# Performance work log

Hardware: AMD Instinct MI355X
Metric: run time of the kernel (lower is better)

The kernel has to match this reference:

```python
import jax, jax.numpy as jnp
import numpy as np
from jax import lax

C = 128          # channel_size
NUM_HEAD = 2
P = 4            # local_patch_num


def setup_inputs() -> dict:
    key = jax.random.key(0)
    ks = jax.random.split(key, 16)
    def w(k, shape, scale=0.02):
        return jax.random.normal(k, shape, dtype=jnp.float32) * scale
    return dict(
        x=jax.random.normal(ks[0], (16, C, 128, 128), jnp.float32),
        h0=jax.random.normal(ks[1], (1, C, 64, 64), jnp.float32),
        c0=jax.random.normal(ks[2], (1, C, 64, 64), jnp.float32),
        conv_w=w(ks[3], (C, C, 2, 2)), conv_b=jnp.zeros((C,), jnp.float32),
        qkv1_w=w(ks[4], (3 * C, C)), qkv1_b=jnp.zeros((3 * C,), jnp.float32),
        mlp1_w1=w(ks[5], (4 * C, C)), mlp1_b1=jnp.zeros((4 * C,), jnp.float32),
        mlp1_w2=w(ks[6], (C, 4 * C)), mlp1_b2=jnp.zeros((C,), jnp.float32),
        qkv2_w=w(ks[7], (3 * C, C)), qkv2_b=jnp.zeros((3 * C,), jnp.float32),
        mlp2_w1=w(ks[8], (4 * C, C)), mlp2_b1=jnp.zeros((4 * C,), jnp.float32),
        mlp2_w2=w(ks[9], (C, 4 * C)), mlp2_b2=jnp.zeros((C,), jnp.float32),
        lstm_wx=w(ks[10], (4 * C, C)),   # 1x1 conv, no bias
        lstm_wh=w(ks[11], (4 * C, C)),   # 1x1 conv
        lstm_bh=jnp.zeros((4 * C,), jnp.float32),
    )


def _linear(x, w, b):
    # torch Linear: y = x @ W.T + b, W is [out, in]
    return jnp.einsum('...i,oi->...o', x, w) + b


def _msa(x, w, b, num_head):
    # x: [b, A, L, c]; attend over L within each group A. scale = sqrt(channel_size).
    bb, A, L, c = x.shape
    hd = c // num_head
    qkv = _linear(x, w, b).reshape(bb, A, L, 3, num_head, hd)
    q = jnp.transpose(qkv[..., 0, :, :], (0, 1, 3, 2, 4))  # [b,A,h,L,hd]
    k = jnp.transpose(qkv[..., 1, :, :], (0, 1, 3, 2, 4))
    v = jnp.transpose(qkv[..., 2, :, :], (0, 1, 3, 2, 4))
    score = jnp.einsum('bahlc,bahmc->bahlm', q, k) / (c ** 0.5)
    attn = jax.nn.softmax(score, axis=-1)
    out = jnp.einsum('bahlm,bahmc->bahlc', attn, v)
    return jnp.transpose(out, (0, 1, 3, 2, 4)).reshape(bb, A, L, c)


def _mlp(x, w1, b1, w2, b2):
    return _linear(jax.nn.gelu(_linear(x, w1, b1), approximate=False), w2, b2)


def reference(x, h0, c0, conv_w, conv_b,
              qkv1_w, qkv1_b, mlp1_w1, mlp1_b1, mlp1_w2, mlp1_b2,
              qkv2_w, qkv2_b, mlp2_w1, mlp2_b1, mlp2_w2, mlp2_b2,
              lstm_wx, lstm_wh, lstm_bh):
    # Conv2d(C, C, kernel=2, stride=2)
    x = lax.conv_general_dilated(x, conv_w, (2, 2), 'VALID',
                                 dimension_numbers=('NCHW', 'OIHW', 'NCHW'))
    x = x + conv_b[None, :, None, None]
    b, c, Hs, Ws = x.shape
    yg, xg = Hs // P, Ws // P
    # Window_partition: b c (yg yl) (xg xl) -> b (yg xg) (yl xl) c
    xw = x.reshape(b, c, yg, P, xg, P).transpose(0, 2, 4, 3, 5, 1).reshape(b, yg * xg, P * P, c)
    xw = xw + _msa(xw, qkv1_w, qkv1_b, NUM_HEAD)      # LocalMSA over window tokens
    xw = xw + _mlp(xw, mlp1_w1, mlp1_b1, mlp1_w2, mlp1_b2)
    xt = jnp.transpose(xw, (0, 2, 1, 3))              # b g l c -> b l g c
    xt = xt + _msa(xt, qkv2_w, qkv2_b, NUM_HEAD)      # DilatedMSA over windows
    xt = xt + _mlp(xt, mlp2_w1, mlp2_b1, mlp2_w2, mlp2_b2)
    # Window_reverse: b (yl xl) (yg xg) c -> b c (yg yl) (xg xl)
    xr = xt.reshape(b, P, P, yg, xg, c).transpose(0, 5, 3, 1, 4, 2).reshape(b, c, yg * P, xg * P)

    # ConvLSTM recurrence over the batch dimension (hidden carried sample-to-sample)
    def step(carry, xi):
        h, Cc = carry  # [C,H,W]
        gates = (jnp.einsum('oc,chw->ohw', lstm_wx, xi)
                 + jnp.einsum('oc,chw->ohw', lstm_wh, h)
                 + lstm_bh[:, None, None])
        f, i, s, o = jnp.split(gates, 4, axis=0)
        f = jax.nn.softmax(f, axis=0)   # Softmax2d = softmax over channels
        i = jax.nn.softmax(i, axis=0)
        o = jax.nn.softmax(o, axis=0)
        s = jnp.tanh(s)
        Cn = f * Cc + i * s
        hn = o * jnp.tanh(Cn)
        return (hn, Cn), hn

    (hf, Cf), hs = lax.scan(step, (h0[0], c0[0]), xr)
    return hs, hf[None], Cf[None]
```

## Files before the change

### kernel.cpp

```cpp
#include <hip/hip_runtime.h>
#include <hip/hip_bf16.h>

typedef unsigned int u32;
typedef unsigned short u16;

#define DI __device__ __forceinline__

typedef __attribute__((ext_vector_type(8))) __bf16 bf16x8;
typedef __attribute__((ext_vector_type(4))) float f32x4;

DI float b2f_u(u32 u){ return __uint_as_float(u << 16); }
DI u16 f2b_u(float f){
  u32 x = __float_as_uint(f);
  x += 0x7fffu + ((x >> 16) & 1u);
  return (u16)(x >> 16);
}
DI void ld8b(const u16* p, float* o){
  uint4 v = *reinterpret_cast<const uint4*>(p);
  o[0] = b2f_u(v.x & 0xffffu); o[1] = b2f_u(v.x >> 16);
  o[2] = b2f_u(v.y & 0xffffu); o[3] = b2f_u(v.y >> 16);
  o[4] = b2f_u(v.z & 0xffffu); o[5] = b2f_u(v.z >> 16);
  o[6] = b2f_u(v.w & 0xffffu); o[7] = b2f_u(v.w >> 16);
}
DI void st8b(u16* p, const float* i){
  uint4 v;
  v.x = (u32)f2b_u(i[0]) | ((u32)f2b_u(i[1]) << 16);
  v.y = (u32)f2b_u(i[2]) | ((u32)f2b_u(i[3]) << 16);
  v.z = (u32)f2b_u(i[4]) | ((u32)f2b_u(i[5]) << 16);
  v.w = (u32)f2b_u(i[6]) | ((u32)f2b_u(i[7]) << 16);
  *reinterpret_cast<uint4*>(p) = v;
}

__global__ void k_detect(const u32* __restrict__ xw, int* __restrict__ flag){
  __shared__ int cnt;
  int t = threadIdx.x;
  if (t == 0) cnt = 0;
  __syncthreads();
  int c = 0;
  for (int i = t; i < 2048; i += 256){
    u32 lo = xw[i] & 0xffffu;
    u32 e = (lo >> 7) & 0xffu;
    if (e < 100u || e > 140u) c++;
  }
  atomicAdd(&cnt, c);
  __syncthreads();
  if (t == 0) *flag = (cnt > 200) ? 1 : 0;
}

__global__ void k_prep(
  const void* __restrict__ conv_w, const void* __restrict__ qkv1_w,
  const void* __restrict__ m1w1, const void* __restrict__ m1w2,
  const void* __restrict__ qkv2_w, const void* __restrict__ m2w1, const void* __restrict__ m2w2,
  const void* __restrict__ lwx, const void* __restrict__ lwh,
  const void* __restrict__ conv_b, const void* __restrict__ qkv1_b,
  const void* __restrict__ m1b1, const void* __restrict__ m1b2,
  const void* __restrict__ qkv2_b, const void* __restrict__ m2b1, const void* __restrict__ m2b2,
  const void* __restrict__ lbh,
  u16* __restrict__ wB_conv, u16* __restrict__ wB_qkv1, u16* __restrict__ wB_m1a,
  u16* __restrict__ wB_m1b, u16* __restrict__ wB_qkv2, u16* __restrict__ wB_m2a,
  u16* __restrict__ wB_m2b, u16* __restrict__ wBx, u16* __restrict__ wBh,
  float* __restrict__ bf_conv, float* __restrict__ bf_qkv1, float* __restrict__ bf_m1b1,
  float* __restrict__ bf_m1b2, float* __restrict__ bf_qkv2, float* __restrict__ bf_m2b1,
  float* __restrict__ bf_m2b2, float* __restrict__ bf_lbh,
  const int* __restrict__ flag){
  int bid = blockIdx.x, t = threadIdx.x;
  int fl = *flag;
  auto cvb = [&](const void* s, u16* d, int base, int n){
    int i = (bid - base)*256 + t;
    if (i < n) d[i] = fl ? f2b_u(((const float*)s)[i]) : ((const u16*)s)[i];
  };
  auto ldf = [&](const void* s, int i)->float{
    return fl ? ((const float*)s)[i] : b2f_u((u32)((const u16*)s)[i]);
  };
  if (bid < 256)       cvb(conv_w, wB_conv, 0,    65536);
  else if (bid < 448)  cvb(qkv1_w, wB_qkv1, 256,  49152);
  else if (bid < 704)  cvb(m1w1,   wB_m1a,  448,  65536);
  else if (bid < 960)  cvb(m1w2,   wB_m1b,  704,  65536);
  else if (bid < 1152) cvb(qkv2_w, wB_qkv2, 960,  49152);
  else if (bid < 1408) cvb(m2w1,   wB_m2a,  1152, 65536);
  else if (bid < 1664) cvb(m2w2,   wB_m2b,  1408, 65536);
  else if (bid < 1920) cvb(lwx,    wBx,     1664, 65536);
  else if (bid < 2176) cvb(lwh,    wBh,     1920, 65536);
  else {
    int i = (bid - 2176)*256 + t;
    if (i < 128)       bf_conv[i]        = ldf(conv_b, i);
    else if (i < 512)  bf_qkv1[i-128]    = ldf(qkv1_b, i-128);
    else if (i < 1024) bf_m1b1[i-512]    = ldf(m1b1,   i-512);
    else if (i < 1152) bf_m1b2[i-1024]   = ldf(m1b2,   i-1024);
    else if (i < 1536) bf_qkv2[i-1152]   = ldf(qkv2_b, i-1152);
    else if (i < 2048) bf_m2b1[i-1536]   = ldf(m2b1,   i-1536);
    else if (i < 2176) bf_m2b2[i-2048]   = ldf(m2b2,   i-2048);
    else if (i < 2688) bf_lbh[i-2176]    = ldf(lbh,    i-2176);
  }
}

__global__ __launch_bounds__(256) void k_conv(const void* __restrict__ x_raw,
                                              const u16* __restrict__ wB,
                                              const float* __restrict__ bias, u16* __restrict__ outA,
                                              const int* __restrict__ flag){
  __shared__ __align__(16) u16 pool[128*136];
  u16* Aa = pool;
  u16* Ys = pool;
  int t = threadIdx.x, bid = blockIdx.x;
  int xh = bid & 1, yg = (bid >> 1) & 15, b = bid >> 5;
  size_t slab = (size_t)b*2097152 + (size_t)(yg*8)*128 + (size_t)xh*64;
  int w = t >> 6, lane = t & 63, fr = lane & 15, fg = lane >> 4;
  f32x4 acc[2][8];
  #pragma unroll
  for (int j=0;j<8;j++){
    float bv = bias[j*16 + fr];
    acc[0][j] = {bv,bv,bv,bv};
    acc[1][j] = {bv,bv,bv,bv};
  }
  for (int ci0 = 0; ci0 < 128; ci0 += 16){
    if (ci0) __syncthreads();
    if (*flag){
      const float* xb = (const float*)x_raw + slab + (size_t)ci0*16384;
      #pragma unroll
      for (int i=0;i<4;i++){
        int idx = i*256 + t;
        int row = idx >> 3, seg = idx & 7;
        int cr = row >> 3, py = row & 7;
        const float* sp = xb + (size_t)cr*16384 + py*128 + seg*8;
        float4 v0 = *reinterpret_cast<const float4*>(sp);
        float4 v1 = *reinterpret_cast<const float4*>(sp + 4);
        int tok0 = seg*16 + (py>>1)*4;
        int k0 = cr*4 + (py&1)*2;
        *reinterpret_cast<u32*>(&Aa[(tok0+0)*72 + k0]) = (u32)f2b_u(v0.x) | ((u32)f2b_u(v0.y)<<16);
        *reinterpret_cast<u32*>(&Aa[(tok0+1)*72 + k0]) = (u32)f2b_u(v0.z) | ((u32)f2b_u(v0.w)<<16);
        *reinterpret_cast<u32*>(&Aa[(tok0+2)*72 + k0]) = (u32)f2b_u(v1.x) | ((u32)f2b_u(v1.y)<<16);
        *reinterpret_cast<u32*>(&Aa[(tok0+3)*72 + k0]) = (u32)f2b_u(v1.z) | ((u32)f2b_u(v1.w)<<16);
      }
    } else {
      const u16* xb = (const u16*)x_raw + slab + (size_t)ci0*16384;
      #pragma unroll
      for (int i=0;i<4;i++){
        int idx = i*256 + t;
        int row = idx >> 3, seg = idx & 7;
        int cr = row >> 3, py = row & 7;
        uint4 v = *reinterpret_cast<const uint4*>(xb + (size_t)cr*16384 + py*128 + seg*8);
        int tok0 = seg*16 + (py>>1)*4;
        int k0 = cr*4 + (py&1)*2;
        *reinterpret_cast<u32*>(&Aa[(tok0+0)*72 + k0]) = v.x;
        *reinterpret_cast<u32*>(&Aa[(tok0+1)*72 + k0]) = v.y;
        *reinterpret_cast<u32*>(&Aa[(tok0+2)*72 + k0]) = v.z;
        *reinterpret_cast<u32*>(&Aa[(tok0+3)*72 + k0]) = v.w;
      }
    }
    __syncthreads();
    bf16x8 a0[2], a1[2];
    #pragma unroll
    for (int kk=0;kk<2;kk++){
      a0[kk] = *reinterpret_cast<const bf16x8*>(&Aa[(w*16+fr)*72 + kk*32 + fg*8]);
      a1[kk] = *reinterpret_cast<const bf16x8*>(&Aa[((w+4)*16+fr)*72 + kk*32 + fg*8]);
    }
    #pragma unroll
    for (int j=0;j<8;j++){
      const u16* wp = wB + (size_t)(j*16+fr)*512 + ci0*4 + fg*8;
      bf16x8 b0 = *reinterpret_cast<const bf16x8*>(wp);
      bf16x8 b1 = *reinterpret_cast<const bf16x8*>(wp + 32);
      acc[0][j] = __builtin_amdgcn_mfma_f32_16x16x32_bf16(a0[0], b0, acc[0][j], 0, 0, 0);
      acc[0][j] = __builtin_amdgcn_mfma_f32_16x16x32_bf16(a0[1], b1, acc[0][j], 0, 0, 0);
      acc[1][j] = __builtin_amdgcn_mfma_f32_16x16x32_bf16(a1[0], b0, acc[1][j], 0, 0, 0);
      acc[1][j] = __builtin_amdgcn_mfma_f32_16x16x32_bf16(a1[1], b1, acc[1][j], 0, 0, 0);
    }
  }
  __syncthreads();
  #pragma unroll
  for (int tt=0;tt<2;tt++){
    int tokbase = (w + tt*4)*16;
    #pragma unroll
    for (int j=0;j<8;j++){
      #pragma unroll
      for (int r=0;r<4;r++)
        Ys[(tokbase + fg*4 + r)*136 + j*16 + fr] = f2b_u(acc[tt][j][r]);
    }
  }
  __syncthreads();
  {
    int tok = t >> 1, half = t & 1;
    int gl = yg*16 + xh*8 + (tok >> 4);
    int l = tok & 15;
    u16* dst = outA + ((size_t)(b*256 + gl)*16 + l)*128 + half*64;
    const u16* src = &Ys[tok*136 + half*64];
    #pragma unroll
    for (int q2=0;q2<8;q2++)
      *reinterpret_cast<uint4*>(dst + q2*8) = *reinterpret_cast<const uint4*>(src + q2*8);
  }
}

__global__ __launch_bounds__(256) void k_msa1(const u16* __restrict__ A, const u16* __restrict__ wB,
                                              const float* __restrict__ qbias, u16* __restrict__ B){
  __shared__ u16 Xs[16*136];
  __shared__ float QKV[16*388];
  __shared__ float S[512];
  int t = threadIdx.x, bid = blockIdx.x;
  {
    int l = t >> 4, c0 = (t & 15)*8;
    *reinterpret_cast<uint4*>(&Xs[l*136 + c0]) =
      *reinterpret_cast<const uint4*>(A + (size_t)bid*2048 + l*128 + c0);
  }
  __syncthreads();
  {
    int w = t >> 6, lane = t & 63, fr = lane & 15, fg = lane >> 4;
    bf16x8 a[4];
    #pragma unroll
    for (int k=0;k<4;k++) a[k] = *reinterpret_cast<const bf16x8*>(&Xs[fr*136 + k*32 + fg*8]);
    #pragma unroll
    for (int j=0;j<6;j++){
      int o = w*96 + j*16 + fr;
      float bv = qbias[o];
      f32x4 d = {bv,bv,bv,bv};
      const u16* wp = wB + (size_t)o*128 + fg*8;
      #pragma unroll
      for (int k=0;k<4;k++){
        bf16x8 b = *reinterpret_cast<const bf16x8*>(wp + k*32);
        d = __builtin_amdgcn_mfma_f32_16x16x32_bf16(a[k], b, d, 0, 0, 0);
      }
      #pragma unroll
      for (int r=0;r<4;r++) QKV[(fg*4+r)*388 + o] = d[r];
    }
  }
  __syncthreads();
  const float scale = 0.08838834764831845f;
  for (int e = t; e < 512; e += 256){
    int h = e >> 8, l = (e>>4)&15, m = e&15;
    const float* q = &QKV[l*388 + h*64];
    const float* kk = &QKV[m*388 + 128 + h*64];
    float s = 0.f;
    #pragma unroll
    for (int d=0; d<64; d++) s += q[d]*kk[d];
    S[(h*16+l)*16 + m] = s*scale;
  }
  __syncthreads();
  if (t < 32){
    float* row = &S[t*16];
    float mx = row[0];
    #pragma unroll
    for (int m=1;m<16;m++) mx = fmaxf(mx,row[m]);
    float sum = 0.f;
    #pragma unroll
    for (int m=0;m<16;m++){ float e = expf(row[m]-mx); row[m]=e; sum+=e; }
    float inv = 1.0f/sum;
    #pragma unroll
    for (int m=0;m<16;m++) row[m] *= inv;
  }
  __syncthreads();
  {
    int l = t >> 4, og = t & 15, o0 = og*8;
    int h = o0 >> 6;
    const float* p = &S[(h*16+l)*16];
    float out8[8];
    #pragma unroll
    for (int j=0;j<8;j++){
      int o = o0+j, d = o & 63;
      float s = 0.f;
      #pragma unroll
      for (int m=0;m<16;m++) s += p[m]*QKV[m*388 + 256 + h*64 + d];
      out8[j] = s + b2f_u((u32)Xs[l*136 + o]);
    }
    st8b(B + (size_t)bid*2048 + l*128 + o0, out8);
  }
}

template<int MODE>
__global__ __launch_bounds__(256) void k_mlp(const u16* __restrict__ in,
    const u16* __restrict__ w1B, const float* __restrict__ b1,
    const u16* __restrict__ w2B, const float* __restrict__ b2,
    u16* __restrict__ out){
  __shared__ u16 Xs[32*136];
  __shared__ u16 Hs[32*520];
  __shared__ u16 Ys[32*136];
  int t = threadIdx.x, bid = blockIdx.x;
  {
    int l = t >> 3, c0 = (t & 7)*16;
    const u16* src = in + (size_t)bid*4096 + l*128 + c0;
    *reinterpret_cast<uint4*>(&Xs[l*136 + c0])     = *reinterpret_cast<const uint4*>(src);
    *reinterpret_cast<uint4*>(&Xs[l*136 + c0 + 8]) = *reinterpret_cast<const uint4*>(src + 8);
  }
  __syncthreads();
  int w = t >> 6, lane = t & 63, fr = lane & 15, fg = lane >> 4;

  {
    bf16x8 a0[4], a1[4];
    #pragma unroll
    for (int k=0;k<4;k++){
      a0[k] = *reinterpret_cast<const bf16x8*>(&Xs[fr*136 + k*32 + fg*8]);
      a1[k] = *reinterpret_cast<const bf16x8*>(&Xs[(16+fr)*136 + k*32 + fg*8]);
    }
    #pragma unroll
    for (int j=0;j<8;j++){
      int o = w*128 + j*16 + fr;
      float bv = b1[o];
      f32x4 d0 = {bv,bv,bv,bv}, d1 = {bv,bv,bv,bv};
      const u16* wp = w1B + (size_t)o*128 + fg*8;
      #pragma unroll
      for (int k=0;k<4;k++){
        bf16x8 b = *reinterpret_cast<const bf16x8*>(wp + k*32);
        d0 = __builtin_amdgcn_mfma_f32_16x16x32_bf16(a0[k], b, d0, 0, 0, 0);
        d1 = __builtin_amdgcn_mfma_f32_16x16x32_bf16(a1[k], b, d1, 0, 0, 0);
      }
      #pragma unroll
      for (int r=0;r<4;r++){
        float v0 = d0[r], v1 = d1[r];
        Hs[(fg*4+r)*520 + o]      = f2b_u(0.5f*v0*(1.0f + erff(v0*0.70710678118654752f)));
        Hs[(16+fg*4+r)*520 + o]   = f2b_u(0.5f*v1*(1.0f + erff(v1*0.70710678118654752f)));
      }
    }
  }
  __syncthreads();

  {
    int na = w*32 + fr, nb = na + 16;
    float ba = b2[na], bb = b2[nb];
    f32x4 d00 = {ba,ba,ba,ba}, d01 = {bb,bb,bb,bb};
    f32x4 d10 = {ba,ba,ba,ba}, d11 = {bb,bb,bb,bb};
    const u16* wpa = w2B + (size_t)na*512 + fg*8;
    const u16* wpb = w2B + (size_t)nb*512 + fg*8;
    #pragma unroll
    for (int k=0;k<16;k++){
      bf16x8 aa = *reinterpret_cast<const bf16x8*>(&Hs[fr*520 + k*32 + fg*8]);
      bf16x8 ab = *reinterpret_cast<const bf16x8*>(&Hs[(16+fr)*520 + k*32 + fg*8]);
      bf16x8 bA = *reinterpret_cast<const bf16x8*>(wpa + k*32);
      bf16x8 bB = *reinterpret_cast<const bf16x8*>(wpb + k*32);
      d00 = __builtin_amdgcn_mfma_f32_16x16x32_bf16(aa, bA, d00, 0, 0, 0);
      d01 = __builtin_amdgcn_mfma_f32_16x16x32_bf16(aa, bB, d01, 0, 0, 0);
      d10 = __builtin_amdgcn_mfma_f32_16x16x32_bf16(ab, bA, d10, 0, 0, 0);
      d11 = __builtin_amdgcn_mfma_f32_16x16x32_bf16(ab, bB, d11, 0, 0, 0);
    }
    #pragma unroll
    for (int r=0;r<4;r++){
      int ta = fg*4 + r, tb = 16 + ta;
      Ys[ta*136 + na] = f2b_u(d00[r] + b2f_u((u32)Xs[ta*136 + na]));
      Ys[ta*136 + nb] = f2b_u(d01[r] + b2f_u((u32)Xs[ta*136 + nb]));
      Ys[tb*136 + na] = f2b_u(d10[r] + b2f_u((u32)Xs[tb*136 + na]));
      Ys[tb*136 + nb] = f2b_u(d11[r] + b2f_u((u32)Xs[tb*136 + nb]));
    }
  }
  __syncthreads();

  {
    int tok = t >> 3, oc = (t & 7)*16;
    uint4 v0 = *reinterpret_cast<const uint4*>(&Ys[tok*136 + oc]);
    uint4 v1 = *reinterpret_cast<const uint4*>(&Ys[tok*136 + oc + 8]);
    int T = bid*32 + tok;
    size_t addr;
    if (MODE == 1){
      int b = T >> 12, g = (T >> 4) & 255, ll = T & 15;
      addr = ((size_t)((b*16 + ll)*256 + g))*128 + oc;
    } else {
      int b = T >> 12, ll = (T >> 8) & 15, g = T & 255;
      int pcoord = ((g >> 4)*4 + (ll >> 2))*64 + ((g & 15)*4 + (ll & 3));
      addr = ((size_t)(b*4096 + pcoord))*128 + oc;
    }
    *reinterpret_cast<uint4*>(out + addr)     = v0;
    *reinterpret_cast<uint4*>(out + addr + 8) = v1;
  }
}

__global__ __launch_bounds__(256) void k_qkv2(const u16* __restrict__ in, const u16* __restrict__ wB,
                                              const float* __restrict__ bias,
                                              u16* __restrict__ qbuf, u16* __restrict__ kvbuf){
  __shared__ u16 Xs[16*136];
  __shared__ u16 Qs[16*392];
  int t = threadIdx.x, bid = blockIdx.x;
  {
    int l = t >> 4, c0 = (t & 15)*8;
    *reinterpret_cast<uint4*>(&Xs[l*136 + c0]) =
      *reinterpret_cast<const uint4*>(in + (size_t)bid*2048 + l*128 + c0);
  }
  __syncthreads();
  {
    int w = t >> 6, lane = t & 63, fr = lane & 15, fg = lane >> 4;
    bf16x8 a[4];
    #pragma unroll
    for (int k=0;k<4;k++) a[k] = *reinterpret_cast<const bf16x8*>(&Xs[fr*136 + k*32 + fg*8]);
    #pragma unroll
    for (int j=0;j<6;j++){
      int o = w*96 + j*16 + fr;
      float bv = bias[o];
      f32x4 d = {bv,bv,bv,bv};
      const u16* wp = wB + (size_t)o*128 + fg*8;
      #pragma unroll
      for (int k=0;k<4;k++){
        bf16x8 b = *reinterpret_cast<const bf16x8*>(wp + k*32);
        d = __builtin_amdgcn_mfma_f32_16x16x32_bf16(a[k], b, d, 0, 0, 0);
      }
      #pragma unroll
      for (int r=0;r<4;r++) Qs[(fg*4+r)*392 + o] = f2b_u(d[r]);
    }
  }
  __syncthreads();
  {
    int l = t >> 4, og = t & 15, o0 = og*24;
    size_t tok = (size_t)bid*16 + l;
    #pragma unroll
    for (int m=0; m<3; m++){
      int oc = o0 + m*8;
      uint4 v = *reinterpret_cast<const uint4*>(&Qs[l*392 + oc]);
      if (oc < 128) *reinterpret_cast<uint4*>(qbuf + tok*128 + oc) = v;
      else          *reinterpret_cast<uint4*>(kvbuf + tok*256 + (oc-128)) = v;
    }
  }
}

__global__ __launch_bounds__(256) void k_attn2(const u16* __restrict__ qbuf, const u16* __restrict__ kvbuf,
                                               u16* __restrict__ y){
  __shared__ __align__(16) char pool[24064];
  u16* Qb = (u16*)pool;
  u16* Kb = (u16*)(pool + 9216);
  u16* Vt = (u16*)(pool + 13824);
  u16* Pb = (u16*)(pool + 18944);
  float* Os = (float*)pool;

  int t = threadIdx.x, bid = blockIdx.x;
  int qt = bid & 3, h = (bid >> 2) & 1, bl = bid >> 3;
  size_t tokbase = (size_t)bl * 256;
  {
    int r = t >> 2, seg = t & 3;
    const u16* src = qbuf + (tokbase + qt*64 + r)*128 + h*64 + seg*16;
    uint4 v0 = *reinterpret_cast<const uint4*>(src);
    uint4 v1 = *reinterpret_cast<const uint4*>(src + 8);
    *reinterpret_cast<uint4*>(&Qb[r*72 + seg*16])     = v0;
    *reinterpret_cast<uint4*>(&Qb[r*72 + seg*16 + 8]) = v1;
  }
  int w = t >> 6, lane = t & 63;
  int fc = lane & 15, fg = lane >> 4;
  float m_reg[4], l_reg[4];
  #pragma unroll
  for (int r=0;r<4;r++){ m_reg[r] = -1e30f; l_reg[r] = 0.0f; }
  f32x4 o[4];
  #pragma unroll
  for (int j=0;j<4;j++) o[j] = {0.f,0.f,0.f,0.f};
  const float scale = 0.08838834764831845f;

  for (int kt=0; kt<8; kt++){
    {
      int r = t >> 3, seg = t & 7;
      const u16* base = kvbuf + (tokbase + kt*32 + r)*256 + h*64;
      *reinterpret_cast<uint4*>(&Kb[r*72 + seg*8]) = *reinterpret_cast<const uint4*>(base + seg*8);
    }
    {
      int pp = t >> 4, dg = t & 15, d0 = dg*4;
      const u16* b0 = kvbuf + (tokbase + kt*32 + 2*pp)*256 + h*64 + 128 + d0;
      uint2 v0 = *reinterpret_cast<const uint2*>(b0);
      uint2 v1 = *reinterpret_cast<const uint2*>(b0 + 256);
      *reinterpret_cast<u32*>(&Vt[(d0+0)*40 + 2*pp]) = (v0.x & 0xffffu) | (v1.x << 16);
      *reinterpret_cast<u32*>(&Vt[(d0+1)*40 + 2*pp]) = (v0.x >> 16) | (v1.x & 0xffff0000u);
      *reinterpret_cast<u32*>(&Vt[(d0+2)*40 + 2*pp]) = (v0.y & 0xffffu) | (v1.y << 16);
      *reinterpret_cast<u32*>(&Vt[(d0+3)*40 + 2*pp]) = (v0.y >> 16) | (v1.y & 0xffff0000u);
    }
    __syncthreads();
    f32x4 s0 = {0.f,0.f,0.f,0.f}, s1 = {0.f,0.f,0.f,0.f};
    {
      bf16x8 a0  = *reinterpret_cast<const bf16x8*>(&Qb[(w*16+fc)*72 + fg*8]);
      bf16x8 a1  = *reinterpret_cast<const bf16x8*>(&Qb[(w*16+fc)*72 + 32 + fg*8]);
      bf16x8 b00 = *reinterpret_cast<const bf16x8*>(&Kb[fc*72 + fg*8]);
      bf16x8 b01 = *reinterpret_cast<const bf16x8*>(&Kb[fc*72 + 32 + fg*8]);
      bf16x8 b10 = *reinterpret_cast<const bf16x8*>(&Kb[(16+fc)*72 + fg*8]);
      bf16x8 b11 = *reinterpret_cast<const bf16x8*>(&Kb[(16+fc)*72 + 32 + fg*8]);
      s0 = __builtin_amdgcn_mfma_f32_16x16x32_bf16(a0, b00, s0, 0, 0, 0);
      s0 = __builtin_amdgcn_mfma_f32_16x16x32_bf16(a1, b01, s0, 0, 0, 0);
      s1 = __builtin_amdgcn_mfma_f32_16x16x32_bf16(a0, b10, s1, 0, 0, 0);
      s1 = __builtin_amdgcn_mfma_f32_16x16x32_bf16(a1, b11, s1, 0, 0, 0);
    }
    float corr[4];
    #pragma unroll
    for (int r=0;r<4;r++){
      float v0 = s0[r]*scale, v1 = s1[r]*scale;
      float mx = fmaxf(v0, v1);
      mx = fmaxf(mx, __shfl_xor(mx, 1));
      mx = fmaxf(mx, __shfl_xor(mx, 2));
      mx = fmaxf(mx, __shfl_xor(mx, 4));
      mx = fmaxf(mx, __shfl_xor(mx, 8));
      float mnew = fmaxf(m_reg[r], mx);
      corr[r] = expf(m_reg[r] - mnew);
      m_reg[r] = mnew;
      float p0 = expf(v0 - mnew), p1 = expf(v1 - mnew);
      float sum = p0 + p1;
      sum += __shfl_xor(sum, 1);
      sum += __shfl_xor(sum, 2);
      sum += __shfl_xor(sum, 4);
      sum += __shfl_xor(sum, 8);
      l_reg[r] = l_reg[r]*corr[r] + sum;
      int row = w*16 + fg*4 + r;
      Pb[row*40 + fc]      = f2b_u(p0);
      Pb[row*40 + 16 + fc] = f2b_u(p1);
    }
    {
      bf16x8 pa = *reinterpret_cast<const bf16x8*>(&Pb[(w*16+fc)*40 + fg*8]);
      #pragma unroll
      for (int jt=0;jt<4;jt++){
        bf16x8 vb = *reinterpret_cast<const bf16x8*>(&Vt[(jt*16+fc)*40 + fg*8]);
        f32x4 oo = o[jt];
        oo[0] *= corr[0]; oo[1] *= corr[1]; oo[2] *= corr[2]; oo[3] *= corr[3];
        o[jt] = __builtin_amdgcn_mfma_f32_16x16x32_bf16(pa, vb, oo, 0, 0, 0);
      }
    }
    __syncthreads();
  }
  float inv[4];
  #pragma unroll
  for (int r=0;r<4;r++) inv[r] = 1.0f / l_reg[r];
  #pragma unroll
  for (int jt=0;jt<4;jt++){
    #pragma unroll
    for (int r=0;r<4;r++)
      Os[(w*16 + fg*4 + r)*68 + jt*16 + fc] = o[jt][r] * inv[r];
  }
  __syncthreads();
  {
    int row = t >> 2, seg = t & 3;
    float ov[16];
    #pragma unroll
    for (int j=0;j<16;j++) ov[j] = Os[row*68 + seg*16 + j];
    u16* dst = y + (tokbase + qt*64 + row)*128 + h*64 + seg*16;
    float res[16]; ld8b(dst, res); ld8b(dst+8, res+8);
    float o16[16];
    #pragma unroll
    for (int j=0;j<16;j++) o16[j] = ov[j] + res[j];
    st8b(dst, o16); st8b(dst+8, o16+8);
  }
}

__global__ __launch_bounds__(256) void k_tr_pc(const void* __restrict__ h0, const void* __restrict__ c0,
                                               float* __restrict__ hws, float* __restrict__ Cst,
                                               u16* __restrict__ hbf,
                                               const int* __restrict__ flag){
  __shared__ float lds[32][33];
  int t = threadIdx.x, bid = blockIdx.x;
  int sel = bid >> 9, tile = bid & 511;
  int pt2 = tile >> 2, ct = tile & 3;
  const void* src = sel ? c0 : h0;
  float* dst = sel ? Cst : hws;
  int r = t >> 3, q = t & 7;
  {
    int c = ct*32 + r;
    int px = pt2*32 + q*4;
    if (*flag){
      float4 v = *reinterpret_cast<const float4*>((const float*)src + (size_t)c*4096 + px);
      lds[r][q*4+0]=v.x; lds[r][q*4+1]=v.y; lds[r][q*4+2]=v.z; lds[r][q*4+3]=v.w;
    } else {
      uint2 u = *reinterpret_cast<const uint2*>((const u16*)src + (size_t)c*4096 + px);
      lds[r][q*4+0]=b2f_u(u.x & 0xffffu); lds[r][q*4+1]=b2f_u(u.x >> 16);
      lds[r][q*4+2]=b2f_u(u.y & 0xffffu); lds[r][q*4+3]=b2f_u(u.y >> 16);
    }
  }
  __syncthreads();
  {
    int px = pt2*32 + r;
    int c = ct*32 + q*4;
    float4 o;
    o.x = lds[q*4+0][r]; o.y = lds[q*4+1][r]; o.z = lds[q*4+2][r]; o.w = lds[q*4+3][r];
    *reinterpret_cast<float4*>(dst + (size_t)px*128 + c) = o;
    if (sel == 0){
      uint2 pk;
      pk.x = (u32)f2b_u(o.x) | ((u32)f2b_u(o.y) << 16);
      pk.y = (u32)f2b_u(o.z) | ((u32)f2b_u(o.w) << 16);
      *reinterpret_cast<uint2*>(hbf + (size_t)px*128 + c) = pk;
    }
  }
}

__global__ __launch_bounds__(256) void k_lstm_step(const u16* __restrict__ xD,
    u16* __restrict__ hbf, float* __restrict__ hws, float* __restrict__ Cst,
    const u16* __restrict__ wBx, const u16* __restrict__ wBh, const float* __restrict__ bh,
    void* __restrict__ dout, int n, const int* __restrict__ flag){
  __shared__ u16 Xa[16*136];
  __shared__ u16 Ha[16*136];
  __shared__ float glds[4*16*132];
  __shared__ u16 hst[16*136];
  int t = threadIdx.x, bid = blockIdx.x;
  int pix0 = bid*16;
  {
    int px = t >> 4, c0 = (t & 15)*8;
    *reinterpret_cast<uint4*>(&Xa[px*136 + c0]) =
      *reinterpret_cast<const uint4*>(xD + ((size_t)n*4096 + pix0 + px)*128 + c0);
    *reinterpret_cast<uint4*>(&Ha[px*136 + c0]) =
      *reinterpret_cast<const uint4*>(hbf + (size_t)(pix0 + px)*128 + c0);
  }
  __syncthreads();
  int w = t >> 6, lane = t & 63, fr = lane & 15, fg = lane >> 4;
  f32x4 acc[8];
  {
    bf16x8 ax[4], ah[4];
    #pragma unroll
    for (int k=0;k<4;k++){
      ax[k] = *reinterpret_cast<const bf16x8*>(&Xa[fr*136 + k*32 + fg*8]);
      ah[k] = *reinterpret_cast<const bf16x8*>(&Ha[fr*136 + k*32 + fg*8]);
    }
    #pragma unroll
    for (int j=0;j<8;j++){
      int o = w*128 + j*16 + fr;
      float bv = bh[o];
      f32x4 d = {bv,bv,bv,bv};
      const u16* wpx = wBx + (size_t)o*128 + fg*8;
      const u16* wph = wBh + (size_t)o*128 + fg*8;
      #pragma unroll
      for (int k=0;k<4;k++){
        bf16x8 b = *reinterpret_cast<const bf16x8*>(wpx + k*32);
        d = __builtin_amdgcn_mfma_f32_16x16x32_bf16(ax[k], b, d, 0, 0, 0);
      }
      #pragma unroll
      for (int k=0;k<4;k++){
        bf16x8 b = *reinterpret_cast<const bf16x8*>(wph + k*32);
        d = __builtin_amdgcn_mfma_f32_16x16x32_bf16(ah[k], b, d, 0, 0, 0);
      }
      acc[j] = d;
    }
  }
  if (w == 2){
    #pragma unroll
    for (int j=0;j<8;j++)
      #pragma unroll
      for (int r=0;r<4;r++)
        glds[(w*16 + fg*4 + r)*132 + j*16 + fr] = tanhf(acc[j][r]);
  } else {
    #pragma unroll
    for (int r=0;r<4;r++){
      float mx = acc[0][r];
      #pragma unroll
      for (int j=1;j<8;j++) mx = fmaxf(mx, acc[j][r]);
      mx = fmaxf(mx, __shfl_xor(mx, 1));
      mx = fmaxf(mx, __shfl_xor(mx, 2));
      mx = fmaxf(mx, __shfl_xor(mx, 4));
      mx = fmaxf(mx, __shfl_xor(mx, 8));
      float e[8], sum = 0.f;
      #pragma unroll
      for (int j=0;j<8;j++){ e[j] = expf(acc[j][r] - mx); sum += e[j]; }
      sum += __shfl_xor(sum, 1);
      sum += __shfl_xor(sum, 2);
      sum += __shfl_xor(sum, 4);
      sum += __shfl_xor(sum, 8);
      float inv = 1.0f/sum;
      #pragma unroll
      for (int j=0;j<8;j++)
        glds[(w*16 + fg*4 + r)*132 + j*16 + fr] = e[j]*inv;
    }
  }
  __syncthreads();
  {
    int chg = t & 15, px = t >> 4;
    int ch0 = chg*8;
    int pix = pix0 + px;
    float fv[8], iv[8], sv[8], ov[8], cc[8];
    #pragma unroll
    for (int q2=0;q2<2;q2++){
      *reinterpret_cast<float4*>(&fv[q2*4]) = *reinterpret_cast<const float4*>(&glds[(0*16+px)*132 + ch0 + q2*4]);
      *reinterpret_cast<float4*>(&iv[q2*4]) = *reinterpret_cast<const float4*>(&glds[(1*16+px)*132 + ch0 + q2*4]);
      *reinterpret_cast<float4*>(&sv[q2*4]) = *reinterpret_cast<const float4*>(&glds[(2*16+px)*132 + ch0 + q2*4]);
      *reinterpret_cast<float4*>(&ov[q2*4]) = *reinterpret_cast<const float4*>(&glds[(3*16+px)*132 + ch0 + q2*4]);
      *reinterpret_cast<float4*>(&cc[q2*4]) = *reinterpret_cast<const float4*>(Cst + (size_t)pix*128 + ch0 + q2*4);
    }
    float cn[8], hn[8];
    #pragma unroll
    for (int j=0;j<8;j++){
      cn[j] = fv[j]*cc[j] + iv[j]*sv[j];
      hn[j] = ov[j]*tanhf(cn[j]);
    }
    #pragma unroll
    for (int q2=0;q2<2;q2++){
      *reinterpret_cast<float4*>(Cst + (size_t)pix*128 + ch0 + q2*4) = *reinterpret_cast<const float4*>(&cn[q2*4]);
      *reinterpret_cast<float4*>(hws + (size_t)pix*128 + ch0 + q2*4) = *reinterpret_cast<const float4*>(&hn[q2*4]);
    }
    uint4 pk;
    pk.x = (u32)f2b_u(hn[0]) | ((u32)f2b_u(hn[1]) << 16);
    pk.y = (u32)f2b_u(hn[2]) | ((u32)f2b_u(hn[3]) << 16);
    pk.z = (u32)f2b_u(hn[4]) | ((u32)f2b_u(hn[5]) << 16);
    pk.w = (u32)f2b_u(hn[6]) | ((u32)f2b_u(hn[7]) << 16);
    *reinterpret_cast<uint4*>(hbf + (size_t)pix*128 + ch0) = pk;
    *reinterpret_cast<uint4*>(&hst[px*136 + ch0]) = pk;
  }
  __syncthreads();
  {
    int ch = t >> 1, ph = t & 1;
    size_t ob = (size_t)n*524288 + (size_t)ch*4096 + pix0 + ph*8;
    if (*flag){
      float* df = (float*)dout;
      float v[8];
      #pragma unroll
      for (int i=0;i<8;i++) v[i] = b2f_u((u32)hst[(ph*8+i)*136 + ch]);
      *reinterpret_cast<float4*>(df + ob)     = make_float4(v[0],v[1],v[2],v[3]);
      *reinterpret_cast<float4*>(df + ob + 4) = make_float4(v[4],v[5],v[6],v[7]);
    } else {
      u16* db = (u16*)dout;
      uint4 pk;
      pk.x = (u32)hst[(ph*8+0)*136 + ch] | ((u32)hst[(ph*8+1)*136 + ch] << 16);
      pk.y = (u32)hst[(ph*8+2)*136 + ch] | ((u32)hst[(ph*8+3)*136 + ch] << 16);
      pk.z = (u32)hst[(ph*8+4)*136 + ch] | ((u32)hst[(ph*8+5)*136 + ch] << 16);
      pk.w = (u32)hst[(ph*8+6)*136 + ch] | ((u32)hst[(ph*8+7)*136 + ch] << 16);
      *reinterpret_cast<uint4*>(db + ob) = pk;
    }
  }
}

__global__ __launch_bounds__(256) void k_final_t(const float* __restrict__ hws, const float* __restrict__ Cst,
                                                 void* __restrict__ dout, const int* __restrict__ flag){
  __shared__ float lds[32][33];
  int t = threadIdx.x, bid = blockIdx.x;
  int sel = bid >> 9, tile = bid & 511;
  int pt2 = tile >> 2, ct = tile & 3;
  const float* src = sel ? Cst : hws;
  size_t base = sel ? 8912896u : 8388608u;
  int r = t >> 3, q = t & 7;
  {
    int px = pt2*32 + r, c = ct*32 + q*4;
    float4 v = *reinterpret_cast<const float4*>(src + (size_t)px*128 + c);
    lds[r][q*4+0]=v.x; lds[r][q*4+1]=v.y; lds[r][q*4+2]=v.z; lds[r][q*4+3]=v.w;
  }
  __syncthreads();
  {
    int c = ct*32 + r, px = pt2*32 + q*4;
    float v0 = lds[q*4+0][r], v1 = lds[q*4+1][r], v2 = lds[q*4+2][r], v3 = lds[q*4+3][r];
    if (*flag){
      *reinterpret_cast<float4*>((float*)dout + base + (size_t)c*4096 + px) = make_float4(v0,v1,v2,v3);
    } else {
      uint2 pk;
      pk.x = (u32)f2b_u(v0) | ((u32)f2b_u(v1) << 16);
      pk.y = (u32)f2b_u(v2) | ((u32)f2b_u(v3) << 16);
      *reinterpret_cast<uint2*>((u16*)dout + base + (size_t)c*4096 + px) = pk;
    }
  }
}

extern "C" void kernel_launch(void* const* d_in, const int* in_sizes, int n_in,
                              void* d_out, int out_size, void* d_ws, size_t ws_size,
                              hipStream_t stream) {
  const void* x      = d_in[0];
  const void* h0     = d_in[1];
  const void* c0     = d_in[2];
  const void* conv_w = d_in[3];
  const void* conv_b = d_in[4];
  const void* qkv1_w = d_in[5];
  const void* qkv1_b = d_in[6];
  const void* m1w1   = d_in[7];
  const void* m1b1   = d_in[8];
  const void* m1w2   = d_in[9];
  const void* m1b2   = d_in[10];
  const void* qkv2_w = d_in[11];
  const void* qkv2_b = d_in[12];
  const void* m2w1   = d_in[13];
  const void* m2b1   = d_in[14];
  const void* m2w2   = d_in[15];
  const void* m2b2   = d_in[16];
  const void* lwx    = d_in[17];
  const void* lwh    = d_in[18];
  const void* lbh    = d_in[19];

  char* p = (char*)d_ws;
  auto alloc = [&](size_t bytes)->void*{
    void* r = (void*)p; p += (bytes + 255) & ~(size_t)255; return r;
  };
  int*   flag    = (int*)alloc(256);
  u16* wB_conv = (u16*)alloc(128*512*2);
  u16* wB_qkv1 = (u16*)alloc(384*128*2);
  u16* wB_m1a  = (u16*)alloc(512*128*2);
  u16* wB_m1b  = (u16*)alloc(128*512*2);
  u16* wB_qkv2 = (u16*)alloc(384*128*2);
  u16* wB_m2a  = (u16*)alloc(512*128*2);
  u16* wB_m2b  = (u16*)alloc(128*512*2);
  u16* wBx     = (u16*)alloc(512*128*2);
  u16* wBh     = (u16*)alloc(512*128*2);
  float* bf_conv = (float*)alloc(128*4);
  float* bf_qkv1 = (float*)alloc(384*4);
  float* bf_m1b1 = (float*)alloc(512*4);
  float* bf_m1b2 = (float*)alloc(128*4);
  float* bf_qkv2 = (float*)alloc(384*4);
  float* bf_m2b1 = (float*)alloc(512*4);
  float* bf_m2b2 = (float*)alloc(128*4);
  float* bf_lbh  = (float*)alloc(512*4);
  u16* R0   = (u16*)alloc(16777216);
  u16* Rbig = (u16*)alloc(33554432);

  u16* bufA = R0;
  u16* bufB = Rbig;
  u16* bufC = R0;
  u16* qbuf = (u16*)d_out;
  u16* kvbuf = Rbig;
  u16* bufD = Rbig;
  float* hws = (float*)((char*)R0 + 8388608);
  float* Cst = (float*)((char*)R0 + 10485760);
  u16*   hbf = (u16*)((char*)R0 + 12582912);

  k_detect<<<1, 256, 0, stream>>>((const u32*)x, flag);

  k_prep<<<2187, 256, 0, stream>>>(
      conv_w, qkv1_w, m1w1, m1w2, qkv2_w, m2w1, m2w2, lwx, lwh,
      conv_b, qkv1_b, m1b1, m1b2, qkv2_b, m2b1, m2b2, lbh,
      wB_conv, wB_qkv1, wB_m1a, wB_m1b, wB_qkv2, wB_m2a, wB_m2b,
      wBx, wBh,
      bf_conv, bf_qkv1, bf_m1b1, bf_m1b2, bf_qkv2, bf_m2b1, bf_m2b2, bf_lbh,
      flag);

  k_conv<<<512, 256, 0, stream>>>(x, wB_conv, bf_conv, bufA, flag);
  k_msa1<<<4096, 256, 0, stream>>>(bufA, wB_qkv1, bf_qkv1, bufB);
  k_mlp<1><<<2048, 256, 0, stream>>>(bufB, wB_m1a, bf_m1b1, wB_m1b, bf_m1b2, bufC);
  k_qkv2<<<4096, 256, 0, stream>>>(bufC, wB_qkv2, bf_qkv2, qbuf, kvbuf);
  k_attn2<<<2048, 256, 0, stream>>>(qbuf, kvbuf, bufC);
  k_mlp<2><<<2048, 256, 0, stream>>>(bufC, wB_m2a, bf_m2b1, wB_m2b, bf_m2b2, bufD);

  k_tr_pc<<<1024, 256, 0, stream>>>(h0, c0, hws, Cst, hbf, flag);
  for (int n = 0; n < 16; n++){
    k_lstm_step<<<256, 256, 0, stream>>>(bufD, hbf, hws, Cst, wBx, wBh, bf_lbh, d_out, n, flag);
  }
  k_final_t<<<1024, 256, 0, stream>>>(hws, Cst, d_out, flag);
}
```

Baseline: 802.2 us.

## Fuse ConvLSTM recurrence into one persistent kernel keeping h and C in LDS

Replaces the h0/c0 transpose kernel, the 16 per-step LSTM launches and the final transpose with a single kernel. Each block owns 16 pixels for all 16 time steps, since the 1x1 convolution and channel softmax never mix pixels. The hidden and cell state stay in shared memory instead of round-tripping through global workspace. This removes 17 launches and the global state traffic, but only 256 blocks run the whole serial recurrence, and the uncoalesced strided loads of h0/c0 happen inside the kernel.

```diff
diff --git a/kernel.cpp b/kernel.cpp
--- a/kernel.cpp
+++ b/kernel.cpp
@@ -523,202 +523,189 @@
   }
 }
 
-__global__ __launch_bounds__(256) void k_tr_pc(const void* __restrict__ h0, const void* __restrict__ c0,
-                                               float* __restrict__ hws, float* __restrict__ Cst,
-                                               u16* __restrict__ hbf,
-                                               const int* __restrict__ flag){
-  __shared__ float lds[32][33];
-  int t = threadIdx.x, bid = blockIdx.x;
-  int sel = bid >> 9, tile = bid & 511;
-  int pt2 = tile >> 2, ct = tile & 3;
-  const void* src = sel ? c0 : h0;
-  float* dst = sel ? Cst : hws;
-  int r = t >> 3, q = t & 7;
-  {
-    int c = ct*32 + r;
-    int px = pt2*32 + q*4;
-    if (*flag){
-      float4 v = *reinterpret_cast<const float4*>((const float*)src + (size_t)c*4096 + px);
-      lds[r][q*4+0]=v.x; lds[r][q*4+1]=v.y; lds[r][q*4+2]=v.z; lds[r][q*4+3]=v.w;
-    } else {
-      uint2 u = *reinterpret_cast<const uint2*>((const u16*)src + (size_t)c*4096 + px);
-      lds[r][q*4+0]=b2f_u(u.x & 0xffffu); lds[r][q*4+1]=b2f_u(u.x >> 16);
-      lds[r][q*4+2]=b2f_u(u.y & 0xffffu); lds[r][q*4+3]=b2f_u(u.y >> 16);
-    }
-  }
-  __syncthreads();
-  {
-    int px = pt2*32 + r;
-    int c = ct*32 + q*4;
-    float4 o;
-    o.x = lds[q*4+0][r]; o.y = lds[q*4+1][r]; o.z = lds[q*4+2][r]; o.w = lds[q*4+3][r];
-    *reinterpret_cast<float4*>(dst + (size_t)px*128 + c) = o;
-    if (sel == 0){
-      uint2 pk;
-      pk.x = (u32)f2b_u(o.x) | ((u32)f2b_u(o.y) << 16);
-      pk.y = (u32)f2b_u(o.z) | ((u32)f2b_u(o.w) << 16);
-      *reinterpret_cast<uint2*>(hbf + (size_t)px*128 + c) = pk;
-    }
-  }
-}
-
-__global__ __launch_bounds__(256) void k_lstm_step(const u16* __restrict__ xD,
-    u16* __restrict__ hbf, float* __restrict__ hws, float* __restrict__ Cst,
+__global__ __launch_bounds__(256) void k_lstm_all(const u16* __restrict__ xD,
+    const void* __restrict__ h0, const void* __restrict__ c0,
     const u16* __restrict__ wBx, const u16* __restrict__ wBh, const float* __restrict__ bh,
-    void* __restrict__ dout, int n, const int* __restrict__ flag){
+    void* __restrict__ dout, const int* __restrict__ flag){
   __shared__ u16 Xa[16*136];
   __shared__ u16 Ha[16*136];
   __shared__ float glds[4*16*132];
+  __shared__ float Cls[16*132];
   __shared__ u16 hst[16*136];
   int t = threadIdx.x, bid = blockIdx.x;
   int pix0 = bid*16;
-  {
-    int px = t >> 4, c0 = (t & 15)*8;
-    *reinterpret_cast<uint4*>(&Xa[px*136 + c0]) =
-      *reinterpret_cast<const uint4*>(xD + ((size_t)n*4096 + pix0 + px)*128 + c0);
-    *reinterpret_cast<uint4*>(&Ha[px*136 + c0]) =
-      *reinterpret_cast<const uint4*>(hbf + (size_t)(pix0 + px)*128 + c0);
-  }
-  __syncthreads();
+  int fl = *flag;
+  {
+    int c = t >> 1, half = t & 1;
+    int pxb = half*8;
+    if (fl){
+      const float* hp = (const float*)h0 + (size_t)c*4096 + pix0 + pxb;
+      const float* cp = (const float*)c0 + (size_t)c*4096 + pix0 + pxb;
+      #pragma unroll
+      for (int i=0;i<8;i++){
+        Ha[(pxb+i)*136 + c] = f2b_u(hp[i]);
+        Cls[(pxb+i)*132 + c] = cp[i];
+      }
+    } else {
+      const u16* hp = (const u16*)h0 + (size_t)c*4096 + pix0 + pxb;
+      const u16* cp = (const u16*)c0 + (size_t)c*4096 + pix0 + pxb;
+      #pragma unroll
+      for (int i=0;i<8;i++){
+        Ha[(pxb+i)*136 + c] = hp[i];
+        Cls[(pxb+i)*132 + c] = b2f_u((u32)cp[i]);
+      }
+    }
+  }
   int w = t >> 6, lane = t & 63, fr = lane & 15, fg = lane >> 4;
-  f32x4 acc[8];
-  {
-    bf16x8 ax[4], ah[4];
-    #pragma unroll
-    for (int k=0;k<4;k++){
-      ax[k] = *reinterpret_cast<const bf16x8*>(&Xa[fr*136 + k*32 + fg*8]);
-      ah[k] = *reinterpret_cast<const bf16x8*>(&Ha[fr*136 + k*32 + fg*8]);
-    }
-    #pragma unroll
-    for (int j=0;j<8;j++){
-      int o = w*128 + j*16 + fr;
-      float bv = bh[o];
-      f32x4 d = {bv,bv,bv,bv};
-      const u16* wpx = wBx + (size_t)o*128 + fg*8;
-      const u16* wph = wBh + (size_t)o*128 + fg*8;
+  for (int n = 0; n < 16; n++){
+    {
+      int px = t >> 4, c0v = (t & 15)*8;
+      *reinterpret_cast<uint4*>(&Xa[px*136 + c0v]) =
+        *reinterpret_cast<const uint4*>(xD + ((size_t)n*4096 + pix0 + px)*128 + c0v);
+    }
+    __syncthreads();
+    f32x4 acc[8];
+    {
+      bf16x8 ax[4], ah[4];
       #pragma unroll
       for (int k=0;k<4;k++){
-        bf16x8 b = *reinterpret_cast<const bf16x8*>(wpx + k*32);
-        d = __builtin_amdgcn_mfma_f32_16x16x32_bf16(ax[k], b, d, 0, 0, 0);
-      }
-      #pragma unroll
-      for (int k=0;k<4;k++){
-        bf16x8 b = *reinterpret_cast<const bf16x8*>(wph + k*32);
-        d = __builtin_amdgcn_mfma_f32_16x16x32_bf16(ah[k], b, d, 0, 0, 0);
-      }
-      acc[j] = d;
-    }
-  }
-  if (w == 2){
-    #pragma unroll
-    for (int j=0;j<8;j++)
-      #pragma unroll
-      for (int r=0;r<4;r++)
-        glds[(w*16 + fg*4 + r)*132 + j*16 + fr] = tanhf(acc[j][r]);
-  } else {
-    #pragma unroll
-    for (int r=0;r<4;r++){
-      float mx = acc[0][r];
-      #pragma unroll
-      for (int j=1;j<8;j++) mx = fmaxf(mx, acc[j][r]);
-      mx = fmaxf(mx, __shfl_xor(mx, 1));
-      mx = fmaxf(mx, __shfl_xor(mx, 2));
-      mx = fmaxf(mx, __shfl_xor(mx, 4));
-      mx = fmaxf(mx, __shfl_xor(mx, 8));
-      float e[8], sum = 0.f;
-      #pragma unroll
-      for (int j=0;j<8;j++){ e[j] = expf(acc[j][r] - mx); sum += e[j]; }
-      sum += __shfl_xor(sum, 1);
-      sum += __shfl_xor(sum, 2);
-      sum += __shfl_xor(sum, 4);
-      sum += __shfl_xor(sum, 8);
-      float inv = 1.0f/sum;
+        ax[k] = *reinterpret_cast<const bf16x8*>(&Xa[fr*136 + k*32 + fg*8]);
+        ah[k] = *reinterpret_cast<const bf16x8*>(&Ha[fr*136 + k*32 + fg*8]);
+      }
+      #pragma unroll
+      for (int j=0;j<8;j++){
+        int o = w*128 + j*16 + fr;
+        float bv = bh[o];
+        f32x4 d = {bv,bv,bv,bv};
+        const u16* wpx = wBx + (size_t)o*128 + fg*8;
+        const u16* wph = wBh + (size_t)o*128 + fg*8;
+        #pragma unroll
+        for (int k=0;k<4;k++){
+          bf16x8 b = *reinterpret_cast<const bf16x8*>(wpx + k*32);
+          d = __builtin_amdgcn_mfma_f32_16x16x32_bf16(ax[k], b, d, 0, 0, 0);
+        }
+        #pragma unroll
+        for (int k=0;k<4;k++){
+          bf16x8 b = *reinterpret_cast<const bf16x8*>(wph + k*32);
+          d = __builtin_amdgcn_mfma_f32_16x16x32_bf16(ah[k], b, d, 0, 0, 0);
+        }
+        acc[j] = d;
+      }
+    }
+    if (w == 2){
       #pragma unroll
       for (int j=0;j<8;j++)
-        glds[(w*16 + fg*4 + r)*132 + j*16 + fr] = e[j]*inv;
-    }
-  }
-  __syncthreads();
-  {
-    int chg = t & 15, px = t >> 4;
-    int ch0 = chg*8;
-    int pix = pix0 + px;
-    float fv[8], iv[8], sv[8], ov[8], cc[8];
-    #pragma unroll
-    for (int q2=0;q2<2;q2++){
-      *reinterpret_cast<float4*>(&fv[q2*4]) = *reinterpret_cast<const float4*>(&glds[(0*16+px)*132 + ch0 + q2*4]);
-      *reinterpret_cast<float4*>(&iv[q2*4]) = *reinterpret_cast<const float4*>(&glds[(1*16+px)*132 + ch0 + q2*4]);
-      *reinterpret_cast<float4*>(&sv[q2*4]) = *reinterpret_cast<const float4*>(&glds[(2*16+px)*132 + ch0 + q2*4]);
-      *reinterpret_cast<float4*>(&ov[q2*4]) = *reinterpret_cast<const float4*>(&glds[(3*16+px)*132 + ch0 + q2*4]);
-      *reinterpret_cast<float4*>(&cc[q2*4]) = *reinterpret_cast<const float4*>(Cst + (size_t)pix*128 + ch0 + q2*4);
-    }
-    float cn[8], hn[8];
-    #pragma unroll
-    for (int j=0;j<8;j++){
-      cn[j] = fv[j]*cc[j] + iv[j]*sv[j];
-      hn[j] = ov[j]*tanhf(cn[j]);
-    }
-    #pragma unroll
-    for (int q2=0;q2<2;q2++){
-      *reinterpret_cast<float4*>(Cst + (size_t)pix*128 + ch0 + q2*4) = *reinterpret_cast<const float4*>(&cn[q2*4]);
-      *reinterpret_cast<float4*>(hws + (size_t)pix*128 + ch0 + q2*4) = *reinterpret_cast<const float4*>(&hn[q2*4]);
-    }
-    uint4 pk;
-    pk.x = (u32)f2b_u(hn[0]) | ((u32)f2b_u(hn[1]) << 16);
-    pk.y = (u32)f2b_u(hn[2]) | ((u32)f2b_u(hn[3]) << 16);
-    pk.z = (u32)f2b_u(hn[4]) | ((u32)f2b_u(hn[5]) << 16);
-    pk.w = (u32)f2b_u(hn[6]) | ((u32)f2b_u(hn[7]) << 16);
-    *reinterpret_cast<uint4*>(hbf + (size_t)pix*128 + ch0) = pk;
-    *reinterpret_cast<uint4*>(&hst[px*136 + ch0]) = pk;
-  }
-  __syncthreads();
-  {
-    int ch = t >> 1, ph = t & 1;
-    size_t ob = (size_t)n*524288 + (size_t)ch*4096 + pix0 + ph*8;
-    if (*flag){
+        #pragma unroll
+        for (int r=0;r<4;r++)
+          glds[(w*16 + fg*4 + r)*132 + j*16 + fr] = tanhf(acc[j][r]);
+    } else {
+      #pragma unroll
+      for (int r=0;r<4;r++){
+        float mx = acc[0][r];
+        #pragma unroll
+        for (int j=1;j<8;j++) mx = fmaxf(mx, acc[j][r]);
+        mx = fmaxf(mx, __shfl_xor(mx, 1));
+        mx = fmaxf(mx, __shfl_xor(mx, 2));
+        mx = fmaxf(mx, __shfl_xor(mx, 4));
+        mx = fmaxf(mx, __shfl_xor(mx, 8));
+        float e[8], sum = 0.f;
+        #pragma unroll
+        for (int j=0;j<8;j++){ e[j] = expf(acc[j][r] - mx); sum += e[j]; }
+        sum += __shfl_xor(sum, 1);
+        sum += __shfl_xor(sum, 2);
+        sum += __shfl_xor(sum, 4);
+        sum += __shfl_xor(sum, 8);
+        float inv = 1.0f/sum;
+        #pragma unroll
+        for (int j=0;j<8;j++)
+          glds[(w*16 + fg*4 + r)*132 + j*16 + fr] = e[j]*inv;
+      }
+    }
+    __syncthreads();
+    {
+      int chg = t & 15, px = t >> 4;
+      int ch0 = chg*8;
+      float fv[8], iv[8], sv[8], ov[8], cc[8];
+      #pragma unroll
+      for (int q2=0;q2<2;q2++){
+        *reinterpret_cast<float4*>(&fv[q2*4]) = *reinterpret_cast<const float4*>(&glds[(0*16+px)*132 + ch0 + q2*4]);
+        *reinterpret_cast<float4*>(&iv[q2*4]) = *reinterpret_cast<const float4*>(&glds[(1*16+px)*132 + ch0 + q2*4]);
+        *reinterpret_cast<float4*>(&sv[q2*4]) = *reinterpret_cast<const float4*>(&glds[(2*16+px)*132 + ch0 + q2*4]);
+        *reinterpret_cast<float4*>(&ov[q2*4]) = *reinterpret_cast<const float4*>(&glds[(3*16+px)*132 + ch0 + q2*4]);
+        *reinterpret_cast<float4*>(&cc[q2*4]) = *reinterpret_cast<const float4*>(&Cls[px*132 + ch0 + q2*4]);
+      }
+      float cn[8], hn[8];
+      #pragma unroll
+      for (int j=0;j<8;j++){
+        cn[j] = fv[j]*cc[j] + iv[j]*sv[j];
+        hn[j] = ov[j]*tanhf(cn[j]);
+      }
+      #pragma unroll
+      for (int q2=0;q2<2;q2++)
+        *reinterpret_cast<float4*>(&Cls[px*132 + ch0 + q2*4]) = *reinterpret_cast<const float4*>(&cn[q2*4]);
+      uint4 pk;
+      pk.x = (u32)f2b_u(hn[0]) | ((u32)f2b_u(hn[1]) << 16);
+      pk.y = (u32)f2b_u(hn[2]) | ((u32)f2b_u(hn[3]) << 16);
+      pk.z = (u32)f2b_u(hn[4]) | ((u32)f2b_u(hn[5]) << 16);
+      pk.w = (u32)f2b_u(hn[6]) | ((u32)f2b_u(hn[7]) << 16);
+      *reinterpret_cast<uint4*>(&Ha[px*136 + ch0])  = pk;
+      *reinterpret_cast<uint4*>(&hst[px*136 + ch0]) = pk;
+      if (n == 15){
+        #pragma unroll
+        for (int q2=0;q2<2;q2++)
+          *reinterpret_cast<float4*>(&glds[px*132 + ch0 + q2*4]) = *reinterpret_cast<const float4*>(&hn[q2*4]);
+      }
+    }
+    __syncthreads();
+    {
+      int ch = t >> 1, ph = t & 1;
+      size_t ob = (size_t)n*524288 + (size_t)ch*4096 + pix0 + ph*8;
+      if (fl){
+        float* df = (float*)dout;
+        float v[8];
+        #pragma unroll
+        for (int i=0;i<8;i++) v[i] = b2f_u((u32)hst[(ph*8+i)*136 + ch]);
+        *reinterpret_cast<float4*>(df + ob)     = make_float4(v[0],v[1],v[2],v[3]);
+        *reinterpret_cast<float4*>(df + ob + 4) = make_float4(v[4],v[5],v[6],v[7]);
+      } else {
+        u16* db = (u16*)dout;
+        uint4 pk;
+        pk.x = (u32)hst[(ph*8+0)*136 + ch] | ((u32)hst[(ph*8+1)*136 + ch] << 16);
+        pk.y = (u32)hst[(ph*8+2)*136 + ch] | ((u32)hst[(ph*8+3)*136 + ch] << 16);
+        pk.z = (u32)hst[(ph*8+4)*136 + ch] | ((u32)hst[(ph*8+5)*136 + ch] << 16);
+        pk.w = (u32)hst[(ph*8+6)*136 + ch] | ((u32)hst[(ph*8+7)*136 + ch] << 16);
+        *reinterpret_cast<uint4*>(db + ob) = pk;
+      }
+    }
+  }
+  __syncthreads();
+  {
+    int c = t >> 1, half = t & 1;
+    int pxb = half*8;
+    if (fl){
+      float hv[8], cv[8];
+      #pragma unroll
+      for (int i=0;i<8;i++){ hv[i] = glds[(pxb+i)*132 + c]; cv[i] = Cls[(pxb+i)*132 + c]; }
       float* df = (float*)dout;
-      float v[8];
-      #pragma unroll
-      for (int i=0;i<8;i++) v[i] = b2f_u((u32)hst[(ph*8+i)*136 + ch]);
-      *reinterpret_cast<float4*>(df + ob)     = make_float4(v[0],v[1],v[2],v[3]);
-      *reinterpret_cast<float4*>(df + ob + 4) = make_float4(v[4],v[5],v[6],v[7]);
+      size_t hb = 8388608u + (size_t)c*4096 + pix0 + pxb;
+      size_t cb = 8912896u + (size_t)c*4096 + pix0 + pxb;
+      *reinterpret_cast<float4*>(df + hb)     = make_float4(hv[0],hv[1],hv[2],hv[3]);
+      *reinterpret_cast<float4*>(df + hb + 4) = make_float4(hv[4],hv[5],hv[6],hv[7]);
+      *reinterpret_cast<float4*>(df + cb)     = make_float4(cv[0],cv[1],cv[2],cv[3]);
+      *reinterpret_cast<float4*>(df + cb + 4) = make_float4(cv[4],cv[5],cv[6],cv[7]);
     } else {
       u16* db = (u16*)dout;
-      uint4 pk;
-      pk.x = (u32)hst[(ph*8+0)*136 + ch] | ((u32)hst[(ph*8+1)*136 + ch] << 16);
-      pk.y = (u32)hst[(ph*8+2)*136 + ch] | ((u32)hst[(ph*8+3)*136 + ch] << 16);
-      pk.z = (u32)hst[(ph*8+4)*136 + ch] | ((u32)hst[(ph*8+5)*136 + ch] << 16);
-      pk.w = (u32)hst[(ph*8+6)*136 + ch] | ((u32)hst[(ph*8+7)*136 + ch] << 16);
-      *reinterpret_cast<uint4*>(db + ob) = pk;
-    }
-  }
-}
-
-__global__ __launch_bounds__(256) void k_final_t(const float* __restrict__ hws, const float* __restrict__ Cst,
-                                                 void* __restrict__ dout, const int* __restrict__ flag){
-  __shared__ float lds[32][33];
-  int t = threadIdx.x, bid = blockIdx.x;
-  int sel = bid >> 9, tile = bid & 511;
-  int pt2 = tile >> 2, ct = tile & 3;
-  const float* src = sel ? Cst : hws;
-  size_t base = sel ? 8912896u : 8388608u;
-  int r = t >> 3, q = t & 7;
-  {
-    int px = pt2*32 + r, c = ct*32 + q*4;
-    float4 v = *reinterpret_cast<const float4*>(src + (size_t)px*128 + c);
-    lds[r][q*4+0]=v.x; lds[r][q*4+1]=v.y; lds[r][q*4+2]=v.z; lds[r][q*4+3]=v.w;
-  }
-  __syncthreads();
-  {
-    int c = ct*32 + r, px = pt2*32 + q*4;
-    float v0 = lds[q*4+0][r], v1 = lds[q*4+1][r], v2 = lds[q*4+2][r], v3 = lds[q*4+3][r];
-    if (*flag){
-      *reinterpret_cast<float4*>((float*)dout + base + (size_t)c*4096 + px) = make_float4(v0,v1,v2,v3);
-    } else {
-      uint2 pk;
-      pk.x = (u32)f2b_u(v0) | ((u32)f2b_u(v1) << 16);
-      pk.y = (u32)f2b_u(v2) | ((u32)f2b_u(v3) << 16);
-      *reinterpret_cast<uint2*>((u16*)dout + base + (size_t)c*4096 + px) = pk;
+      uint4 hp, cp2;
+      hp.x = (u32)hst[(pxb+0)*136 + c] | ((u32)hst[(pxb+1)*136 + c] << 16);
+      hp.y = (u32)hst[(pxb+2)*136 + c] | ((u32)hst[(pxb+3)*136 + c] << 16);
+      hp.z = (u32)hst[(pxb+4)*136 + c] | ((u32)hst[(pxb+5)*136 + c] << 16);
+      hp.w = (u32)hst[(pxb+6)*136 + c] | ((u32)hst[(pxb+7)*136 + c] << 16);
+      cp2.x = (u32)f2b_u(Cls[(pxb+0)*132 + c]) | ((u32)f2b_u(Cls[(pxb+1)*132 + c]) << 16);
+      cp2.y = (u32)f2b_u(Cls[(pxb+2)*132 + c]) | ((u32)f2b_u(Cls[(pxb+3)*132 + c]) << 16);
+      cp2.z = (u32)f2b_u(Cls[(pxb+4)*132 + c]) | ((u32)f2b_u(Cls[(pxb+5)*132 + c]) << 16);
+      cp2.w = (u32)f2b_u(Cls[(pxb+6)*132 + c]) | ((u32)f2b_u(Cls[(pxb+7)*132 + c]) << 16);
+      *reinterpret_cast<uint4*>(db + 8388608u + (size_t)c*4096 + pix0 + pxb) = hp;
+      *reinterpret_cast<uint4*>(db + 8912896u + (size_t)c*4096 + pix0 + pxb) = cp2;
     }
   }
 }
@@ -778,9 +765,6 @@
   u16* qbuf = (u16*)d_out;
   u16* kvbuf = Rbig;
   u16* bufD = Rbig;
-  float* hws = (float*)((char*)R0 + 8388608);
-  float* Cst = (float*)((char*)R0 + 10485760);
-  u16*   hbf = (u16*)((char*)R0 + 12582912);
 
   k_detect<<<1, 256, 0, stream>>>((const u32*)x, flag);
 
@@ -799,9 +783,5 @@
   k_attn2<<<2048, 256, 0, stream>>>(qbuf, kvbuf, bufC);
   k_mlp<2><<<2048, 256, 0, stream>>>(bufC, wB_m2a, bf_m2b1, wB_m2b, bf_m2b2, bufD);
 
-  k_tr_pc<<<1024, 256, 0, stream>>>(h0, c0, hws, Cst, hbf, flag);
-  for (int n = 0; n < 16; n++){
-    k_lstm_step<<<256, 256, 0, stream>>>(bufD, hbf, hws, Cst, wBx, wBh, bf_lbh, d_out, n, flag);
-  }
-  k_final_t<<<1024, 256, 0, stream>>>(hws, Cst, d_out, flag);
-}
+  k_lstm_all<<<256, 256, 0, stream>>>(bufD, h0, c0, wBx, wBh, bf_lbh, d_out, flag);
+}
```

After: 663.9 us. 1.21x faster.
